# Kernel tuning notes

Measured on AMD Instinct MI355X. Metric: run time of the kernel, lower is better.

## Reference

```python
import jax, jax.numpy as jnp
import numpy as np


def layer_norm(x, w, b, eps=1e-5):
    mu = jnp.mean(x, axis=-1, keepdims=True)
    var = jnp.mean(jnp.square(x - mu), axis=-1, keepdims=True)
    return (x - mu) / jnp.sqrt(var + eps) * w + b


def setup_inputs() -> dict:
    B, T, S, D, K = 8, 2048, 2048, 512, 3
    ks = jax.random.split(jax.random.key(0), 8)
    w_scale = 0.02  # modest init so softmax/layernorm stay in a sane range
    return {
        "x": jax.random.normal(ks[0], (B, T, D), jnp.float32),
        "enc": jax.random.normal(ks[1], (B, S, D), jnp.float32),
        "conv_w": jax.random.normal(ks[2], (2 * D, D, K), jnp.float32) * w_scale,
        "conv_b": jnp.zeros((2 * D,), jnp.float32),
        "ln1_w": jnp.ones((D,), jnp.float32),
        "ln1_b": jnp.zeros((D,), jnp.float32),
        "Wq": jax.random.normal(ks[3], (D, D), jnp.float32) * w_scale,
        "bq": jnp.zeros((D,), jnp.float32),
        "Wk": jax.random.normal(ks[4], (D, D), jnp.float32) * w_scale,
        "bk": jnp.zeros((D,), jnp.float32),
        "Wv": jax.random.normal(ks[5], (D, D), jnp.float32) * w_scale,
        "bv": jnp.zeros((D,), jnp.float32),
        "Wo": jax.random.normal(ks[6], (D, D), jnp.float32) * w_scale,
        "bo": jnp.zeros((D,), jnp.float32),
        "ln2_w": jnp.ones((D,), jnp.float32),
        "ln2_b": jnp.zeros((D,), jnp.float32),
    }


def reference(x, enc, conv_w, conv_b, ln1_w, ln1_b, Wq, bq, Wk, bk, Wv, bv, Wo, bo, ln2_w, ln2_b):
    D = x.shape[-1]
    K = conv_w.shape[-1]
    # Causal GLU: left-pad by K-1 so each output sees only past/current positions.
    xt = jnp.transpose(x, (0, 2, 1))  # [B, D, T]
    xt = jnp.pad(xt, ((0, 0), (0, 0), (K - 1, 0)))
    conv = jax.lax.conv_general_dilated(
        xt, conv_w, window_strides=(1,), padding="VALID",
        dimension_numbers=("NCH", "OIH", "NCH"))
    conv = conv + conv_b[None, :, None]
    conv = jnp.transpose(conv, (0, 2, 1))  # [B, T, 2D]
    a, g = jnp.split(conv, 2, axis=-1)
    glu = a * jax.nn.sigmoid(g)
    # residual + LN1 (dropout is identity in eval mode)
    h = layer_norm(glu + x, ln1_w, ln1_b)
    # cross-attention: bmm -> softmax -> bmm (single head)
    q = h @ Wq.T + bq            # [B, T, D]
    k = enc @ Wk.T + bk          # [B, S, D]
    v = enc @ Wv.T + bv          # [B, S, D]
    scores = jnp.einsum("btd,bsd->bts", q, k) / jnp.sqrt(jnp.float32(D))
    attn = jax.nn.softmax(scores, axis=-1)  # [B, T, S]
    ctx = jnp.einsum("bts,bsd->btd", attn, v)
    ctx = ctx @ Wo.T + bo
    out = layer_norm(h + ctx, ln2_w, ln2_b)
    return out, attn
```

## Files before the change

kernel.cpp:

```cpp
#include <hip/hip_runtime.h>
#include <hip/hip_bf16.h>
#include <stdint.h>


typedef unsigned short ushortT;
typedef __bf16 bf16x8 __attribute__((ext_vector_type(8)));
typedef float floatx4 __attribute__((ext_vector_type(4)));
typedef unsigned short ushort4v __attribute__((ext_vector_type(4)));
typedef unsigned short ushort8 __attribute__((ext_vector_type(8)));

__device__ __forceinline__ ushortT f2bf(float f) {
  unsigned u = __builtin_bit_cast(unsigned, f);
  u += 0x7FFFu + ((u >> 16) & 1u);
  return (ushortT)(u >> 16);
}
__device__ __forceinline__ float bf2f(ushortT u) {
  return __builtin_bit_cast(float, (unsigned)u << 16);
}

__device__ __forceinline__ void gload_lds16(const void* g, void* l) {
  __builtin_amdgcn_global_load_lds(
      (const __attribute__((address_space(1))) void*)g,
      (__attribute__((address_space(3))) void*)l, 16, 0, 0);
}

__global__ __launch_bounds__(256)
void k_f32_to_bf16v(const float* __restrict__ src, ushortT* __restrict__ dst, long n4) {
  long i = (long)blockIdx.x * 256 + threadIdx.x;
  if (i >= n4) return;
  floatx4 v = *(const floatx4*)&src[i * 4];
  ushort4v o;
#pragma unroll
  for (int j = 0; j < 4; j++) o[j] = f2bf(v[j]);
  *(ushort4v*)&dst[i * 4] = o;
}

__global__ __launch_bounds__(256)
void k_w4(const float* __restrict__ w0, const float* __restrict__ w1,
          const float* __restrict__ w2, const float* __restrict__ w3,
          ushortT* __restrict__ dst) {
  long i = (long)blockIdx.x * 256 + threadIdx.x;
  int m = (int)(i >> 16);
  long within = (i & 65535) * 4;
  const float* s = (m == 0) ? w0 : (m == 1) ? w1 : (m == 2) ? w2 : w3;
  floatx4 v = *(const floatx4*)&s[within];
  ushort4v o;
#pragma unroll
  for (int j = 0; j < 4; j++) o[j] = f2bf(v[j]);
  *(ushort4v*)&dst[(long)m * 262144 + within] = o;
}

__global__ __launch_bounds__(128)
void k_xpad(const float* __restrict__ x, ushortT* __restrict__ xp) {
  int row = blockIdx.x;
  int b = row / 2050, tp = row % 2050;
  int c = threadIdx.x * 4;
  ushort4v o = {0, 0, 0, 0};
  if (tp >= 2) {
    floatx4 v = *(const floatx4*)&x[((long)(b * 2048 + tp - 2)) * 512 + c];
#pragma unroll
    for (int j = 0; j < 4; j++) o[j] = f2bf(v[j]);
  }
  *(ushort4v*)&xp[(long)row * 512 + c] = o;
}

__global__ __launch_bounds__(256)
void k_convw(const float* __restrict__ w, ushortT* __restrict__ dst) {
  long idx = (long)blockIdx.x * 256 + threadIdx.x;
  if (idx >= 1024L * 1536) return;
  int n = (int)(idx / 1536), kk = (int)(idx % 1536);
  int tap = kk >> 9, i = kk & 511;
  int o = ((n >> 4) & 1) * 512 + (n >> 5) * 16 + (n & 15);
  dst[idx] = f2bf(w[(o * 512 + i) * 3 + tap]);
}

template<int CONV_A, int GLU, int BIAS, int WBF16, int DUALZ, int SWAP>
__global__ __launch_bounds__(512)
void k_gemm256(const ushortT* __restrict__ A, const ushortT* __restrict__ A2, int lda, long aBatch,
               const ushortT* __restrict__ Bm, const ushortT* __restrict__ Bm2, int ldb, long bBatch,
               const float* __restrict__ bias, const float* __restrict__ bias2,
               const float* __restrict__ xres,
               float* __restrict__ Cf, ushortT* __restrict__ Cb, ushortT* __restrict__ Cb2,
               long cBatch, int ldc, int Kdim, float scale)
{
  __shared__ ushortT lds[2][2 * 16384];

  const int tid  = threadIdx.x;
  const int lane = tid & 63;
  const int wave = tid >> 6;
  const int wr   = wave >> 2;
  const int wc   = wave & 3;
  const int l15  = lane & 15;
  const int quad = lane >> 4;

  const ushortT* Ap = A;
  const ushortT* Bp = Bm;
  const float* biasP = bias;
  ushortT* CbP = Cb;
  if (DUALZ && blockIdx.z) { Ap = A2; Bp = Bm2; biasP = bias2; CbP = Cb2; }
  const long zA = DUALZ ? 0 : (long)blockIdx.z * aBatch;
  const long zB = DUALZ ? 0 : (long)blockIdx.z * bBatch;
  const long zC = DUALZ ? 0 : (long)blockIdx.z * cBatch;
  const int rowBase = (SWAP ? blockIdx.y : blockIdx.x) * 256;
  const int colBase = (SWAP ? blockIdx.x : blockIdx.y) * 256;

  auto STAGE_A = [&](int t, int l) {
    ushortT* sA = lds[t & 1];
    const int k0 = t << 6;
    int idx = l * 512 + tid;
    int row = idx >> 3;
    int ck  = ((tid & 7) ^ (row & 7)) << 3;
    if (CONV_A) {
      int gr = rowBase + row;
      int gc = k0 + ck;
      int tap = gc >> 9, ii = gc & 511;
      int b = gr >> 11, tt = gr & 2047;
      long gofs = ((long)(b * 2050 + tt + tap) << 9) + ii;
      gload_lds16(Ap + gofs, sA + idx * 8);
    } else {
      long gofs = zA + (long)(rowBase + row) * lda + (k0 + ck);
      gload_lds16(Ap + gofs, sA + idx * 8);
    }
  };
  auto STAGE_B = [&](int t, int l) {
    ushortT* sB = lds[t & 1] + 16384;
    const int k0 = t << 6;
    int idx = l * 512 + tid;
    int row = idx >> 3;
    int ck  = ((tid & 7) ^ (row & 7)) << 3;
    long gofs = zB + (long)(colBase + row) * ldb + (k0 + ck);
    gload_lds16(Bp + gofs, sB + idx * 8);
  };

  auto LD = [&](const ushortT* s, int r, int c) -> bf16x8 {
    return *(const bf16x8*)&s[r * 64 + ((c ^ (r & 7)) << 3)];
  };

  floatx4 zero = {0.f, 0.f, 0.f, 0.f};
  floatx4 acc[8][4];
#pragma unroll
  for (int mi = 0; mi < 8; mi++)
#pragma unroll
    for (int ni = 0; ni < 4; ni++) acc[mi][ni] = zero;

  const int NT = Kdim >> 6;
#pragma unroll
  for (int l = 0; l < 4; l++) { STAGE_B(0, l); }
#pragma unroll
  for (int l = 0; l < 4; l++) { STAGE_A(0, l); }
#pragma unroll
  for (int l = 0; l < 4; l++) { STAGE_B(1, l); }
#pragma unroll
  for (int l = 0; l < 4; l++) { STAGE_A(1, l); }

  for (int t = 0; t < NT; t++) {
    if (t < NT - 1) asm volatile("s_waitcnt vmcnt(8)" ::: "memory");
    else            asm volatile("s_waitcnt vmcnt(0)" ::: "memory");
    __builtin_amdgcn_s_barrier();

    const ushortT* sA = lds[t & 1];
    const ushortT* sB = sA + 16384;

    bf16x8 av[4][2], bv[4][2];
#pragma unroll
    for (int ni = 0; ni < 4; ni++)
#pragma unroll
      for (int ks = 0; ks < 2; ks++)
        bv[ni][ks] = LD(sB, wc * 64 + ni * 16 + l15, ks * 4 + quad);
#pragma unroll
    for (int mi = 0; mi < 4; mi++)
#pragma unroll
      for (int ks = 0; ks < 2; ks++)
        av[mi][ks] = LD(sA, wr * 128 + mi * 16 + l15, ks * 4 + quad);

    __builtin_amdgcn_s_setprio(1);
#pragma unroll
    for (int mi = 0; mi < 4; mi++)
#pragma unroll
      for (int ni = 0; ni < 4; ni++)
#pragma unroll
        for (int ks = 0; ks < 2; ks++)
          acc[mi][ni] = __builtin_amdgcn_mfma_f32_16x16x32_bf16(av[mi][ks], bv[ni][ks], acc[mi][ni], 0, 0, 0);
    __builtin_amdgcn_s_setprio(0);

    __builtin_amdgcn_s_barrier();

#pragma unroll
    for (int mi = 0; mi < 4; mi++)
#pragma unroll
      for (int ks = 0; ks < 2; ks++)
        av[mi][ks] = LD(sA, wr * 128 + 64 + mi * 16 + l15, ks * 4 + quad);

    if (t + 2 < NT) {
      STAGE_B(t + 2, 0); STAGE_B(t + 2, 1); STAGE_B(t + 2, 2); STAGE_B(t + 2, 3);
      STAGE_A(t + 2, 0); STAGE_A(t + 2, 2);
    }

    __builtin_amdgcn_s_setprio(1);
#pragma unroll
    for (int mi = 0; mi < 4; mi++)
#pragma unroll
      for (int ni = 0; ni < 4; ni++)
#pragma unroll
        for (int ks = 0; ks < 2; ks++)
          acc[4 + mi][ni] = __builtin_amdgcn_mfma_f32_16x16x32_bf16(av[mi][ks], bv[ni][ks], acc[4 + mi][ni], 0, 0, 0);
    __builtin_amdgcn_s_setprio(0);

    __builtin_amdgcn_s_barrier();
    if (t + 2 < NT) { STAGE_A(t + 2, 1); STAGE_A(t + 2, 3); }
  }

  if (GLU) {
#pragma unroll
    for (int mi = 0; mi < 8; mi++) {
#pragma unroll
      for (int ni = 0; ni < 4; ni += 2) {
        int colA = colBase + wc * 64 + ni * 16;
        int d = (colA >> 5) * 16 + l15;
        float ba = biasP[d], bg = biasP[512 + d];
#pragma unroll
        for (int r = 0; r < 4; r++) {
          int grow = rowBase + wr * 128 + mi * 16 + quad * 4 + r;
          float a = acc[mi][ni][r] + ba;
          float g = acc[mi][ni + 1][r] + bg;
          float val = a / (1.0f + __expf(-g)) + xres[(long)grow * 512 + d];
          Cf[(long)grow * 512 + d] = val;
        }
      }
    }
  } else {
#pragma unroll
    for (int mi = 0; mi < 8; mi++) {
#pragma unroll
      for (int ni = 0; ni < 4; ni++) {
        int gcol = colBase + wc * 64 + ni * 16 + l15;
        float bcol = BIAS ? biasP[gcol] : 0.0f;
#pragma unroll
        for (int r = 0; r < 4; r++) {
          int grow = rowBase + wr * 128 + mi * 16 + quad * 4 + r;
          float val = acc[mi][ni][r] * scale + bcol;
          long off = zC + (long)grow * ldc + gcol;
          if (WBF16) CbP[off] = f2bf(val);
          else       Cf[off] = val;
        }
      }
    }
  }
}

__global__ __launch_bounds__(512)
void k_ctx128(const ushortT* __restrict__ P,
              const ushortT* __restrict__ vT,
              ushortT* __restrict__ ctxb)
{
  __shared__ ushortT lds[2][(128 + 256) * 64];

  const int tid  = threadIdx.x;
  const int lane = tid & 63;
  const int wave = tid >> 6;
  const int wr   = wave >> 2;
  const int wc   = wave & 3;
  const int l15  = lane & 15;
  const int quad = lane >> 4;

  const int lid = blockIdx.x;
  const int z   = lid & 7;
  const int idx = lid >> 3;
  const int rowBase = (idx >> 1) * 128;
  const int colBase = (idx & 1) * 256;
  const long zA = (long)z * 2048 * 2048;

  auto STAGE = [&](int t) {
    ushortT* sA = lds[t & 1];
    ushortT* sB = sA + 128 * 64;
    const int k0 = t << 6;
#pragma unroll
    for (int l = 0; l < 2; l++) {
      int i2 = l * 512 + tid;
      int row = i2 >> 3;
      int ck  = ((tid & 7) ^ (row & 7)) << 3;
      long gofs = zA + (long)(rowBase + row) * 2048 + (k0 + ck);
      gload_lds16(P + gofs, sA + i2 * 8);
    }
#pragma unroll
    for (int l = 0; l < 4; l++) {
      int i2 = l * 512 + tid;
      int row = i2 >> 3;
      int ck  = ((tid & 7) ^ (row & 7)) << 3;
      long gofs = (long)(colBase + row) * 16384 + (long)z * 2048 + (k0 + ck);
      gload_lds16(vT + gofs, sB + i2 * 8);
    }
  };

  auto LD = [&](const ushortT* s, int r, int c) -> bf16x8 {
    return *(const bf16x8*)&s[r * 64 + ((c ^ (r & 7)) << 3)];
  };

  floatx4 zero = {0.f, 0.f, 0.f, 0.f};
  floatx4 acc[4][4];
#pragma unroll
  for (int mi = 0; mi < 4; mi++)
#pragma unroll
    for (int ni = 0; ni < 4; ni++) acc[mi][ni] = zero;

  const int NT = 32;
  STAGE(0);
  STAGE(1);

  for (int t = 0; t < NT; t++) {
    if (t < NT - 1) asm volatile("s_waitcnt vmcnt(6)" ::: "memory");
    else            asm volatile("s_waitcnt vmcnt(0)" ::: "memory");
    __builtin_amdgcn_s_barrier();

    const ushortT* sA = lds[t & 1];
    const ushortT* sB = sA + 128 * 64;

    bf16x8 av[4][2], bv[4][2];
#pragma unroll
    for (int ni = 0; ni < 4; ni++)
#pragma unroll
      for (int ks = 0; ks < 2; ks++)
        bv[ni][ks] = LD(sB, wc * 64 + ni * 16 + l15, ks * 4 + quad);
#pragma unroll
    for (int mi = 0; mi < 4; mi++)
#pragma unroll
      for (int ks = 0; ks < 2; ks++)
        av[mi][ks] = LD(sA, wr * 64 + mi * 16 + l15, ks * 4 + quad);

    __builtin_amdgcn_s_setprio(1);
#pragma unroll
    for (int mi = 0; mi < 4; mi++)
#pragma unroll
      for (int ni = 0; ni < 4; ni++)
#pragma unroll
        for (int ks = 0; ks < 2; ks++)
          acc[mi][ni] = __builtin_amdgcn_mfma_f32_16x16x32_bf16(av[mi][ks], bv[ni][ks], acc[mi][ni], 0, 0, 0);
    __builtin_amdgcn_s_setprio(0);

    __builtin_amdgcn_s_barrier();
    if (t + 2 < NT) STAGE(t + 2);
  }

#pragma unroll
  for (int mi = 0; mi < 4; mi++) {
#pragma unroll
    for (int ni = 0; ni < 4; ni++) {
      int col = colBase + wc * 64 + ni * 16 + l15;
#pragma unroll
      for (int r = 0; r < 4; r++) {
        long grow = (long)z * 2048 + rowBase + wr * 64 + mi * 16 + quad * 4 + r;
        ctxb[grow * 512 + col] = f2bf(acc[mi][ni][r]);
      }
    }
  }
}

template<int BIAS, int WBF16, int LNEPI>
__global__ __launch_bounds__(512)
void k_gemm64(const ushortT* __restrict__ A, int lda, long aBatch,
              const ushortT* __restrict__ Bm, int ldb, long bBatch,
              const float* __restrict__ bias, const ushortT* __restrict__ hres,
              const float* __restrict__ lnw, const float* __restrict__ lnb,
              float* __restrict__ Cf, ushortT* __restrict__ Cb,
              long cBatch, int ldc, int Kdim, float scale)
{
  __shared__ ushortT lds[2][(64 + 512) * 64];

  const int tid  = threadIdx.x;
  const int lane = tid & 63;
  const int wave = tid >> 6;
  const int l15  = lane & 15;
  const int quad = lane >> 4;

  const long zA = (long)blockIdx.z * aBatch;
  const long zB = (long)blockIdx.z * bBatch;
  const long zC = (long)blockIdx.z * cBatch;
  const int rowBase = blockIdx.y * 64;
  const int colBase = blockIdx.x * 512;

  auto STAGE = [&](int t) {
    ushortT* sA = lds[t & 1];
    ushortT* sB = sA + 64 * 64;
    const int k0 = t << 6;
    {
      int row = tid >> 3;
      int ck  = ((tid & 7) ^ (row & 7)) << 3;
      long gofs = zA + (long)(rowBase + row) * lda + (k0 + ck);
      gload_lds16(A + gofs, sA + tid * 8);
    }
#pragma unroll
    for (int l = 0; l < 8; l++) {
      int idx = l * 512 + tid;
      int row = idx >> 3;
      int ck  = ((tid & 7) ^ (row & 7)) << 3;
      long gofs = zB + (long)(colBase + row) * ldb + (k0 + ck);
      gload_lds16(Bm + gofs, sB + idx * 8);
    }
  };

  auto LD = [&](const ushortT* s, int r, int c) -> bf16x8 {
    return *(const bf16x8*)&s[r * 64 + ((c ^ (r & 7)) << 3)];
  };

  floatx4 zero = {0.f, 0.f, 0.f, 0.f};
  floatx4 acc[4][4];
#pragma unroll
  for (int mi = 0; mi < 4; mi++)
#pragma unroll
    for (int ni = 0; ni < 4; ni++) acc[mi][ni] = zero;

  const int NT = Kdim >> 6;
  STAGE(0);
  STAGE(1);

  for (int t = 0; t < NT; t++) {
    if (t < NT - 1) asm volatile("s_waitcnt vmcnt(9)" ::: "memory");
    else            asm volatile("s_waitcnt vmcnt(0)" ::: "memory");
    __builtin_amdgcn_s_barrier();

    const ushortT* sA = lds[t & 1];
    const ushortT* sB = sA + 64 * 64;

    bf16x8 av[4][2], bv[4][2];
#pragma unroll
    for (int ni = 0; ni < 4; ni++)
#pragma unroll
      for (int ks = 0; ks < 2; ks++)
        bv[ni][ks] = LD(sB, wave * 64 + ni * 16 + l15, ks * 4 + quad);
#pragma unroll
    for (int mi = 0; mi < 4; mi++)
#pragma unroll
      for (int ks = 0; ks < 2; ks++)
        av[mi][ks] = LD(sA, mi * 16 + l15, ks * 4 + quad);

    __builtin_amdgcn_s_setprio(1);
#pragma unroll
    for (int mi = 0; mi < 4; mi++)
#pragma unroll
      for (int ni = 0; ni < 4; ni++)
#pragma unroll
        for (int ks = 0; ks < 2; ks++)
          acc[mi][ni] = __builtin_amdgcn_mfma_f32_16x16x32_bf16(av[mi][ks], bv[ni][ks], acc[mi][ni], 0, 0, 0);
    __builtin_amdgcn_s_setprio(0);

    __builtin_amdgcn_s_barrier();
    if (t + 2 < NT) STAGE(t + 2);
  }

  if (LNEPI) {
    float bov[4], lw[4], lb[4];
#pragma unroll
    for (int ni = 0; ni < 4; ni++) {
      int col = wave * 64 + ni * 16 + l15;
      bov[ni] = bias[col]; lw[ni] = lnw[col]; lb[ni] = lnb[col];
    }
    float* psum = (float*)&lds[0][0];
    float* pssq = psum + 8 * 64;
    __syncthreads();
#pragma unroll
    for (int mi = 0; mi < 4; mi++) {
#pragma unroll
      for (int r = 0; r < 4; r++) {
        int rowl = mi * 16 + quad * 4 + r;
        long grow = rowBase + rowl;
        float ps = 0.f, pq = 0.f;
#pragma unroll
        for (int ni = 0; ni < 4; ni++) {
          int col = wave * 64 + ni * 16 + l15;
          float val = acc[mi][ni][r] + bov[ni] + bf2f(hres[grow * 512 + col]);
          acc[mi][ni][r] = val;
          ps += val; pq += val * val;
        }
#pragma unroll
        for (int off = 1; off < 16; off <<= 1) { ps += __shfl_xor(ps, off); pq += __shfl_xor(pq, off); }
        if (l15 == 0) { psum[wave * 64 + rowl] = ps; pssq[wave * 64 + rowl] = pq; }
      }
    }
    __syncthreads();
#pragma unroll
    for (int mi = 0; mi < 4; mi++) {
#pragma unroll
      for (int r = 0; r < 4; r++) {
        int rowl = mi * 16 + quad * 4 + r;
        float S = 0.f, Q = 0.f;
#pragma unroll
        for (int w = 0; w < 8; w++) { S += psum[w * 64 + rowl]; Q += pssq[w * 64 + rowl]; }
        float mu = S * (1.0f / 512.0f);
        float rstd = rsqrtf(Q * (1.0f / 512.0f) - mu * mu + 1e-5f);
        long grow = rowBase + rowl;
#pragma unroll
        for (int ni = 0; ni < 4; ni++) {
          int col = wave * 64 + ni * 16 + l15;
          Cf[grow * 512 + col] = (acc[mi][ni][r] - mu) * rstd * lw[ni] + lb[ni];
        }
      }
    }
  } else {
#pragma unroll
    for (int mi = 0; mi < 4; mi++) {
#pragma unroll
      for (int ni = 0; ni < 4; ni++) {
        int gcol = colBase + wave * 64 + ni * 16 + l15;
        float bcol = (BIAS == 1) ? bias[gcol] : 0.0f;
#pragma unroll
        for (int r = 0; r < 4; r++) {
          int grow = rowBase + mi * 16 + quad * 4 + r;
          float val = acc[mi][ni][r] * scale + bcol + ((BIAS == 2) ? bias[grow] : 0.0f);
          long off = zC + (long)grow * ldc + gcol;
          if (WBF16) Cb[off] = f2bf(val);
          else       Cf[off] = val;
        }
      }
    }
  }
}

__global__ __launch_bounds__(128)
void k_ln(const float* __restrict__ src, const float* __restrict__ w, const float* __restrict__ b,
          ushortT* __restrict__ outb)
{
  __shared__ float s1[2], s2[2];
  long r = blockIdx.x;
  int tid = threadIdx.x;
  floatx4 v = *(const floatx4*)&src[r * 512 + tid * 4];
  float sum = v[0] + v[1] + v[2] + v[3];
  float ssq = v[0]*v[0] + v[1]*v[1] + v[2]*v[2] + v[3]*v[3];
#pragma unroll
  for (int off = 32; off; off >>= 1) { sum += __shfl_xor(sum, off); ssq += __shfl_xor(ssq, off); }
  if ((tid & 63) == 0) { s1[tid >> 6] = sum; s2[tid >> 6] = ssq; }
  __syncthreads();
  sum = s1[0] + s1[1]; ssq = s2[0] + s2[1];
  float mu = sum * (1.0f / 512.0f);
  float var = ssq * (1.0f / 512.0f) - mu * mu;
  float rstd = rsqrtf(var + 1e-5f);
  floatx4 wv = *(const floatx4*)&w[tid * 4];
  floatx4 bv = *(const floatx4*)&b[tid * 4];
  ushort4v ob;
#pragma unroll
  for (int j = 0; j < 4; j++) ob[j] = f2bf((v[j] - mu) * rstd * wv[j] + bv[j]);
  *(ushort4v*)&outb[r * 512 + tid * 4] = ob;
}

__global__ __launch_bounds__(256)
void k_softmax(ushortT* __restrict__ logits, float* __restrict__ attn)
{
  __shared__ float sred[4];
  long r = blockIdx.x;
  ushortT* lrow = logits + r * 2048;
  float* arow = attn + r * 2048;
  int tid = threadIdx.x;
  ushort8 uv = *(const ushort8*)&lrow[tid * 8];
  float v[8];
#pragma unroll
  for (int j = 0; j < 8; j++) v[j] = bf2f(uv[j]);
  float mx = v[0];
#pragma unroll
  for (int j = 1; j < 8; j++) mx = fmaxf(mx, v[j]);
#pragma unroll
  for (int off = 32; off; off >>= 1) mx = fmaxf(mx, __shfl_xor(mx, off));
  if ((tid & 63) == 0) sred[tid >> 6] = mx;
  __syncthreads();
  mx = fmaxf(fmaxf(sred[0], sred[1]), fmaxf(sred[2], sred[3]));
  __syncthreads();
  float sum = 0.f;
#pragma unroll
  for (int j = 0; j < 8; j++) { v[j] = __expf(v[j] - mx); sum += v[j]; }
#pragma unroll
  for (int off = 32; off; off >>= 1) sum += __shfl_xor(sum, off);
  if ((tid & 63) == 0) sred[tid >> 6] = sum;
  __syncthreads();
  sum = sred[0] + sred[1] + sred[2] + sred[3];
  float inv = 1.0f / sum;
  floatx4 o0, o1;
  ushort8 ob;
#pragma unroll
  for (int j = 0; j < 8; j++) {
    float p = v[j] * inv;
    if (j < 4) o0[j] = p; else o1[j - 4] = p;
    ob[j] = f2bf(p);
  }
  *(floatx4*)&arow[tid * 8] = o0;
  *(floatx4*)&arow[tid * 8 + 4] = o1;
  *(ushort8*)&lrow[tid * 8] = ob;
}

extern "C" void kernel_launch(void* const* d_in, const int* in_sizes, int n_in,
                              void* d_out, int out_size, void* d_ws, size_t ws_size,
                              hipStream_t stream)
{
  const float* x      = (const float*)d_in[0];
  const float* enc    = (const float*)d_in[1];
  const float* conv_w = (const float*)d_in[2];
  const float* conv_b = (const float*)d_in[3];
  const float* ln1_w  = (const float*)d_in[4];
  const float* ln1_b  = (const float*)d_in[5];
  const float* Wq     = (const float*)d_in[6];
  const float* bq     = (const float*)d_in[7];
  const float* Wk     = (const float*)d_in[8];
  const float* bk     = (const float*)d_in[9];
  const float* Wv     = (const float*)d_in[10];
  const float* bv     = (const float*)d_in[11];
  const float* Wo     = (const float*)d_in[12];
  const float* bo     = (const float*)d_in[13];
  const float* ln2_w  = (const float*)d_in[14];
  const float* ln2_b  = (const float*)d_in[15];

  const long BT = 16384, Dd = 512, S = 2048, TT = 2048;
  float* out  = (float*)d_out;
  float* attn = out + BT * Dd;

  char* p = (char*)d_ws;
  auto alloc = [&](size_t bytes) { char* r = p; p += (bytes + 255) & ~255UL; return r; };
  float*   hglu  = (float*)alloc(BT * Dd * 4);
  ushortT* xpad  = (ushortT*)alloc(8L * 2050 * 512 * 2);
  ushortT* encbf = (ushortT*)alloc(BT * Dd * 2);
  ushortT* hbf   = (ushortT*)alloc(BT * Dd * 2);
  ushortT* qbf   = (ushortT*)alloc(BT * Dd * 2);
  ushortT* kbf   = (ushortT*)alloc(BT * Dd * 2);
  ushortT* vT    = (ushortT*)alloc(Dd * BT * 2);
  ushortT* ctxbf = (ushortT*)alloc(BT * Dd * 2);
  ushortT* sl    = (ushortT*)alloc(BT * S * 2);
  ushortT* Wcbf  = (ushortT*)alloc(1024L * 1536 * 2);
  ushortT* wall  = (ushortT*)alloc(4L * 262144 * 2);
  ushortT* Wqbf = wall, *Wkbf = wall + 262144, *Wvbf = wall + 2 * 262144, *Wobf = wall + 3 * 262144;

  k_xpad<<<8 * 2050, 128, 0, stream>>>(x, xpad);
  k_f32_to_bf16v<<<(BT * Dd / 4 + 255) / 256, 256, 0, stream>>>(enc, encbf, BT * Dd / 4);
  k_convw<<<(1024 * 1536 + 255) / 256, 256, 0, stream>>>(conv_w, Wcbf);
  k_w4<<<1024, 256, 0, stream>>>(Wq, Wk, Wv, Wo, wall);

  k_gemm256<1, 1, 0, 0, 0, 0><<<dim3(64, 4, 1), 512, 0, stream>>>(
      xpad, nullptr, 0, 0, Wcbf, nullptr, 1536, 0,
      conv_b, nullptr, x, hglu, nullptr, nullptr, 0, 512, 1536, 1.0f);
  k_ln<<<16384, 128, 0, stream>>>(hglu, ln1_w, ln1_b, hbf);

  k_gemm256<0, 0, 1, 1, 1, 0><<<dim3(64, 2, 2), 512, 0, stream>>>(
      hbf, encbf, 512, 0, Wqbf, Wkbf, 512, 0,
      bq, bk, nullptr, nullptr, qbf, kbf, 0, 512, 512, 1.0f);

  k_gemm64<2, 1, 0><<<dim3(32, 8, 1), 512, 0, stream>>>(
      Wvbf, 512, 0, encbf, 512, 0,
      bv, nullptr, nullptr, nullptr,
      nullptr, vT, 0, 16384, 512, 1.0f);

  k_gemm256<0, 0, 0, 1, 0, 0><<<dim3(8, 8, 8), 512, 0, stream>>>(
      qbf, nullptr, 512, TT * Dd, kbf, nullptr, 512, S * Dd,
      nullptr, nullptr, nullptr, nullptr, sl, nullptr,
      TT * S, 2048, 512, 0.04419417382415922f);
  k_softmax<<<16384, 256, 0, stream>>>(sl, attn);

  k_ctx128<<<256, 512, 0, stream>>>(sl, vT, ctxbf);

  k_gemm64<0, 0, 1><<<dim3(1, 256, 1), 512, 0, stream>>>(
      ctxbf, 512, 0, Wobf, 512, 0,
      bo, hbf, ln2_w, ln2_b,
      out, nullptr, 0, 512, 512, 1.0f);
}
```

Before: 499.4 us.

## Split GEMM main loop into four MFMA phases with interleaved staging

Restructures the bf16 GEMM inner loop into four k-half phases separated by barriers, interleaving global-to-LDS staging of the next tile between MFMA groups in a ping-pong style schedule. The vmcnt wait moves from the loop top to just before staging A, and the first tile's wait is hoisted before the loop. This aims to overlap memory traffic with matrix math more evenly. It adds many more barriers per iteration, and correctness depends on the vmcnt counts matching the staging order.

```diff
diff --git a/kernel.cpp b/kernel.cpp
--- a/kernel.cpp
+++ b/kernel.cpp
@@ -145,23 +145,21 @@
 
   const int NT = Kdim >> 6;
 #pragma unroll
-  for (int l = 0; l < 4; l++) { STAGE_B(0, l); }
-#pragma unroll
-  for (int l = 0; l < 4; l++) { STAGE_A(0, l); }
-#pragma unroll
-  for (int l = 0; l < 4; l++) { STAGE_B(1, l); }
-#pragma unroll
-  for (int l = 0; l < 4; l++) { STAGE_A(1, l); }
+  for (int l = 0; l < 4; l++) STAGE_B(0, l);
+#pragma unroll
+  for (int l = 0; l < 4; l++) STAGE_A(0, l);
+#pragma unroll
+  for (int l = 0; l < 4; l++) STAGE_B(1, l);
+#pragma unroll
+  for (int l = 0; l < 4; l++) STAGE_A(1, l);
+  asm volatile("s_waitcnt vmcnt(8)" ::: "memory");
+  __builtin_amdgcn_s_barrier();
 
   for (int t = 0; t < NT; t++) {
-    if (t < NT - 1) asm volatile("s_waitcnt vmcnt(8)" ::: "memory");
-    else            asm volatile("s_waitcnt vmcnt(0)" ::: "memory");
-    __builtin_amdgcn_s_barrier();
-
     const ushortT* sA = lds[t & 1];
     const ushortT* sB = sA + 16384;
 
-    bf16x8 av[4][2], bv[4][2];
+    bf16x8 bv[4][2], av[4][2];
 #pragma unroll
     for (int ni = 0; ni < 4; ni++)
 #pragma unroll
@@ -172,42 +170,58 @@
 #pragma unroll
       for (int ks = 0; ks < 2; ks++)
         av[mi][ks] = LD(sA, wr * 128 + mi * 16 + l15, ks * 4 + quad);
-
+    __builtin_amdgcn_s_barrier();
+    asm volatile("s_waitcnt lgkmcnt(0)" ::: "memory");
     __builtin_amdgcn_s_setprio(1);
 #pragma unroll
     for (int mi = 0; mi < 4; mi++)
 #pragma unroll
       for (int ni = 0; ni < 4; ni++)
-#pragma unroll
-        for (int ks = 0; ks < 2; ks++)
-          acc[mi][ni] = __builtin_amdgcn_mfma_f32_16x16x32_bf16(av[mi][ks], bv[ni][ks], acc[mi][ni], 0, 0, 0);
+        acc[mi][ni] = __builtin_amdgcn_mfma_f32_16x16x32_bf16(av[mi][0], bv[ni][0], acc[mi][ni], 0, 0, 0);
     __builtin_amdgcn_s_setprio(0);
-
-    __builtin_amdgcn_s_barrier();
-
+    __builtin_amdgcn_s_barrier();
+
+    if (t + 2 < NT) { STAGE_B(t + 2, 0); STAGE_B(t + 2, 1); }
+    __builtin_amdgcn_s_barrier();
+    __builtin_amdgcn_s_setprio(1);
+#pragma unroll
+    for (int mi = 0; mi < 4; mi++)
+#pragma unroll
+      for (int ni = 0; ni < 4; ni++)
+        acc[mi][ni] = __builtin_amdgcn_mfma_f32_16x16x32_bf16(av[mi][1], bv[ni][1], acc[mi][ni], 0, 0, 0);
+    __builtin_amdgcn_s_setprio(0);
+    __builtin_amdgcn_s_barrier();
+
+    bf16x8 a2[4][2];
 #pragma unroll
     for (int mi = 0; mi < 4; mi++)
 #pragma unroll
       for (int ks = 0; ks < 2; ks++)
-        av[mi][ks] = LD(sA, wr * 128 + 64 + mi * 16 + l15, ks * 4 + quad);
-
-    if (t + 2 < NT) {
-      STAGE_B(t + 2, 0); STAGE_B(t + 2, 1); STAGE_B(t + 2, 2); STAGE_B(t + 2, 3);
-      STAGE_A(t + 2, 0); STAGE_A(t + 2, 2);
-    }
-
+        a2[mi][ks] = LD(sA, wr * 128 + 64 + mi * 16 + l15, ks * 4 + quad);
+    if (t + 2 < NT) { STAGE_B(t + 2, 2); STAGE_B(t + 2, 3); }
+    __builtin_amdgcn_s_barrier();
+    asm volatile("s_waitcnt lgkmcnt(0)" ::: "memory");
     __builtin_amdgcn_s_setprio(1);
 #pragma unroll
     for (int mi = 0; mi < 4; mi++)
 #pragma unroll
       for (int ni = 0; ni < 4; ni++)
-#pragma unroll
-        for (int ks = 0; ks < 2; ks++)
-          acc[4 + mi][ni] = __builtin_amdgcn_mfma_f32_16x16x32_bf16(av[mi][ks], bv[ni][ks], acc[4 + mi][ni], 0, 0, 0);
+        acc[4 + mi][ni] = __builtin_amdgcn_mfma_f32_16x16x32_bf16(a2[mi][0], bv[ni][0], acc[4 + mi][ni], 0, 0, 0);
     __builtin_amdgcn_s_setprio(0);
-
-    __builtin_amdgcn_s_barrier();
-    if (t + 2 < NT) { STAGE_A(t + 2, 1); STAGE_A(t + 2, 3); }
+    __builtin_amdgcn_s_barrier();
+
+    if (t + 2 < NT)      { asm volatile("s_waitcnt vmcnt(4)" ::: "memory"); }
+    else if (t + 1 < NT) { asm volatile("s_waitcnt vmcnt(0)" ::: "memory"); }
+    if (t + 2 < NT) { STAGE_A(t + 2, 0); STAGE_A(t + 2, 2); STAGE_A(t + 2, 1); STAGE_A(t + 2, 3); }
+    __builtin_amdgcn_s_barrier();
+    __builtin_amdgcn_s_setprio(1);
+#pragma unroll
+    for (int mi = 0; mi < 4; mi++)
+#pragma unroll
+      for (int ni = 0; ni < 4; ni++)
+        acc[4 + mi][ni] = __builtin_amdgcn_mfma_f32_16x16x32_bf16(a2[mi][1], bv[ni][1], acc[4 + mi][ni], 0, 0, 0);
+    __builtin_amdgcn_s_setprio(0);
+    __builtin_amdgcn_s_barrier();
   }
 
   if (GLU) {
```

Result: no change. 507.6 us (+1.6%).
